# Kernel optimization log

Hardware: AMD Instinct MI355X
Metric: run time of the kernel (lower is better)

## Reference

```python
import jax, jax.numpy as jnp
import numpy as np

D = 256  # MCB sketch/output dimension


def count_sketch(x, h, s, d=D):
    # x: [B,H,W,C] channel-last; h: [C] int hash indices in [0,d); s: [C] +/-1 signs
    xs = x * s
    return jnp.zeros(x.shape[:-1] + (d,), x.dtype).at[..., h].add(xs)


def mcb(x, y, h1, s1, h2, s2, d=D):
    # Compact bilinear pooling per spatial location. x,y: [B,C,H,W] -> [B,d,H,W]
    xt = jnp.moveaxis(x, 1, -1)
    yt = jnp.moveaxis(y, 1, -1)
    fx = jnp.fft.rfft(count_sketch(xt, h1, s1, d), axis=-1)
    fy = jnp.fft.rfft(count_sketch(yt, h2, s2, d), axis=-1)
    out = jnp.fft.irfft(fx * fy, n=d, axis=-1)  # circular convolution of the two sketches
    return jnp.moveaxis(out, -1, 1)


def setup_inputs() -> dict:
    key = jax.random.key(0)
    ks = jax.random.split(key, 10)
    B, C, H, W, ATTR = 64, 256, 28, 28, 300
    entity_feature = jax.random.normal(ks[0], (B, C, H, W), jnp.float32)
    attr_one_hot = jax.random.uniform(ks[1], (B, ATTR), jnp.float32)
    W_emb = jax.random.normal(ks[2], (C, ATTR), jnp.float32) * 0.05
    b_emb = jax.random.normal(ks[3], (C,), jnp.float32) * 0.01
    h1 = jax.random.randint(ks[4], (C,), 0, D, jnp.int32)
    h2 = jax.random.randint(ks[5], (C,), 0, D, jnp.int32)
    s1 = jnp.where(jax.random.bernoulli(ks[6], 0.5, (C,)), 1.0, -1.0).astype(jnp.float32)
    s2 = jnp.where(jax.random.bernoulli(ks[7], 0.5, (C,)), 1.0, -1.0).astype(jnp.float32)
    conv1_w = jax.random.normal(ks[8], (32, C), jnp.float32) * 0.05
    conv2_w = jax.random.normal(ks[9], (1, 32), jnp.float32) * 0.05
    return {"entity_feature": entity_feature, "attr_one_hot": attr_one_hot,
            "W_emb": W_emb, "b_emb": b_emb, "h1": h1, "s1": s1, "h2": h2, "s2": s2,
            "conv1_w": conv1_w, "conv2_w": conv2_w}


def reference(entity_feature, attr_one_hot, W_emb, b_emb, h1, s1, h2, s2, conv1_w, conv2_w):
    # textual embedding: Linear(attr_num -> 256)
    emb = attr_one_hot @ W_emb.T + b_emb                      # [B,256]
    attr = jnp.broadcast_to(emb[:, :, None, None], entity_feature.shape)  # expand_as
    mcb_feat = mcb(attr, entity_feature, h1, s1, h2, s2)      # [B,256,H,W]
    hidden = jax.nn.relu(jnp.einsum('bchw,oc->bohw', mcb_feat, conv1_w))  # conv1x1 256->32
    attr_map = jax.nn.sigmoid(jnp.einsum('bchw,oc->bohw', hidden, conv2_w))  # conv1x1 32->1
    attr_feature = attr_map * entity_feature
    return attr_map, attr_feature
```

## Files before the change

### kernel.cpp

```cpp
#include <hip/hip_runtime.h>
#include <math.h>

#define BATCH 64
#define CC    256
#define ATTRN 300
#define DD    256
#define HW    784
#define HW4   196
#define O1    32
#define TF4   49


__global__ __launch_bounds__(256) void k1_emb_sketch(
    const float* __restrict__ attr_one_hot,
    const float* __restrict__ W_emb,
    const float* __restrict__ b_emb,
    const int*   __restrict__ h1,
    const float* __restrict__ s1,
    float* __restrict__ sx)
{
    const int b = blockIdx.x, t = threadIdx.x;
    __shared__ float s_attr[ATTRN];
    __shared__ float s_W[256 * 36];
    __shared__ float s_sx[DD];

    s_attr[t] = attr_one_hot[b * ATTRN + t];
    if (t < ATTRN - 256) s_attr[256 + t] = attr_one_hot[b * ATTRN + 256 + t];
    s_sx[t] = 0.f;

    float acc = b_emb[t];
    for (int a0 = 0; a0 < ATTRN; a0 += 32) {
        __syncthreads();
        const int ncol = (ATTRN - a0) < 32 ? (ATTRN - a0) : 32;
        const int nf4 = ncol >> 2;
        for (int i = t; i < 256 * nf4; i += 256) {
            int r = i / nf4, v = i - r * nf4;
            float4 w = *(const float4*)(W_emb + r * ATTRN + a0 + 4 * v);
            *(float4*)(&s_W[r * 36 + 4 * v]) = w;
        }
        __syncthreads();
        for (int v = 0; v < nf4; ++v) {
            float4 wv = *(const float4*)(&s_W[t * 36 + 4 * v]);
            float4 av = *(const float4*)(&s_attr[a0 + 4 * v]);
            acc += av.x * wv.x + av.y * wv.y + av.z * wv.z + av.w * wv.w;
        }
    }
    __syncthreads();
    atomicAdd(&s_sx[h1[t]], acc * s1[t]);
    __syncthreads();
    sx[b * DD + t] = s_sx[t];
}

__global__ __launch_bounds__(256) void k2_corr(
    const float* __restrict__ sx,
    const float* __restrict__ conv1_w,
    float* __restrict__ corrT)
{
    const int b = blockIdx.x, og = blockIdx.y, t = threadIdx.x;
    const int o0 = og * 8;
    __shared__ float s_sx[DD];
    __shared__ float s_w1[8][DD];
    __shared__ float s_c[8][DD];

    s_sx[t] = sx[b * DD + t];
#pragma unroll
    for (int j = 0; j < 8; ++j) s_w1[j][t] = conv1_w[(o0 + j) * CC + t];
    __syncthreads();

    float acc[8] = {0.f,0.f,0.f,0.f,0.f,0.f,0.f,0.f};
    for (int k4 = 0; k4 < 64; ++k4) {
        const int k = k4 * 4;
        float x0 = s_sx[(k     - t) & 255];
        float x1 = s_sx[(k + 1 - t) & 255];
        float x2 = s_sx[(k + 2 - t) & 255];
        float x3 = s_sx[(k + 3 - t) & 255];
#pragma unroll
        for (int oo = 0; oo < 8; ++oo) {
            float4 w = *(const float4*)&s_w1[oo][k];
            acc[oo] += w.x * x0 + w.y * x1 + w.z * x2 + w.w * x3;
        }
    }
#pragma unroll
    for (int oo = 0; oo < 8; ++oo) s_c[oo][t] = acc[oo];
    __syncthreads();

    float4 r0, r1;
    r0.x = s_c[0][t]; r0.y = s_c[1][t]; r0.z = s_c[2][t]; r0.w = s_c[3][t];
    r1.x = s_c[4][t]; r1.y = s_c[5][t]; r1.z = s_c[6][t]; r1.w = s_c[7][t];
    float4* dst = (float4*)(corrT + ((size_t)b * DD + t) * O1 + o0);
    dst[0] = r0; dst[1] = r1;
}

#define FMA4(A, S, E) { (A).x += (S)*(E).x; (A).y += (S)*(E).y; (A).z += (S)*(E).z; (A).w += (S)*(E).w; }

__global__ __launch_bounds__(1024, 4) void k3_main(
    const float* __restrict__ ent,
    const float* __restrict__ corrT,
    const int*   __restrict__ h2,
    const float* __restrict__ s2,
    const float* __restrict__ conv2_w,
    float* __restrict__ out_map,
    float* __restrict__ out_feat)
{
    const int b = blockIdx.x, tile = blockIdx.y;
    const int tid  = threadIdx.x;
    const int wv   = tid >> 6, lane = tid & 63;
    const int ci   = wv >> 2;
    const int oi   = wv & 3;

    union SMem {
        float  Pl[CC][36];
        float4 red[4][TF4][9];
    };
    __shared__ SMem sm;
    __shared__ float4 s_amap4[TF4];
    __shared__ float  s_c2[O1];

    {
        const int c = tid >> 2, qp = tid & 3;
        const int hc = h2[c];
        const float sc = s2[c];
        const float4* src = (const float4*)(corrT + ((size_t)b * DD + hc) * O1);
        float4 x0 = src[2 * qp], x1 = src[2 * qp + 1];
        x0.x *= sc; x0.y *= sc; x0.z *= sc; x0.w *= sc;
        x1.x *= sc; x1.y *= sc; x1.z *= sc; x1.w *= sc;
        *(float4*)&sm.Pl[c][8 * qp]     = x0;
        *(float4*)&sm.Pl[c][8 * qp + 4] = x1;
        if (tid < O1) s_c2[tid] = conv2_w[tid];
    }
    __syncthreads();

    const bool act = lane < TF4;
    const int f4i = tile * TF4 + (act ? lane : TF4 - 1);
    const float4* ent4 = (const float4*)ent;
    const int c0 = ci * 64;

    float4 acc[8];
#pragma unroll
    for (int o = 0; o < 8; ++o) acc[o] = make_float4(0.f, 0.f, 0.f, 0.f);

    const float4* eptr = ent4 + (size_t)(b * CC + c0) * HW4 + f4i;
#pragma unroll 4
    for (int cc = 0; cc < 64; ++cc) {
        const int c = c0 + cc;
        float4 e4 = eptr[(size_t)cc * HW4];
        float4 pa = *(const float4*)&sm.Pl[c][8 * oi];
        float4 pb = *(const float4*)&sm.Pl[c][8 * oi + 4];
        FMA4(acc[0], pa.x, e4); FMA4(acc[1], pa.y, e4);
        FMA4(acc[2], pa.z, e4); FMA4(acc[3], pa.w, e4);
        FMA4(acc[4], pb.x, e4); FMA4(acc[5], pb.y, e4);
        FMA4(acc[6], pb.z, e4); FMA4(acc[7], pb.w, e4);
    }

    float pre = 0.f;
#pragma unroll
    for (int g = 0; g < 4; ++g) {
        __syncthreads();
        if (oi == g && act) {
#pragma unroll
            for (int i = 0; i < 8; ++i) sm.red[ci][lane][i] = acc[i];
        }
        __syncthreads();
        if (tid < 4 * TF4) {
            const int fi = tid >> 2, j = tid & 3;
#pragma unroll
            for (int i = 0; i < 8; ++i) {
                float v = ((const float*)&sm.red[0][fi][i])[j]
                        + ((const float*)&sm.red[1][fi][i])[j]
                        + ((const float*)&sm.red[2][fi][i])[j]
                        + ((const float*)&sm.red[3][fi][i])[j];
                pre += s_c2[8 * g + i] * fmaxf(v, 0.f);
            }
        }
    }
    __syncthreads();
    if (tid < 4 * TF4) {
        const int fi = tid >> 2, j = tid & 3;
        float am = 1.f / (1.f + expf(-pre));
        ((float*)&s_amap4[fi])[j] = am;
        out_map[b * HW + tile * (4 * TF4) + tid] = am;
    }
    __syncthreads();

    const float4 am4 = s_amap4[act ? lane : 0];
    float4* of4 = (float4*)out_feat;
    const int cb = wv * 16;
#pragma unroll 4
    for (int cc = 0; cc < 16; ++cc) {
        const int c = cb + cc;
        if (act) {
            const size_t idx = (size_t)(b * CC + c) * HW4 + f4i;
            float4 e4 = ent4[idx];
            float4 r;
            r.x = am4.x * e4.x; r.y = am4.y * e4.y;
            r.z = am4.z * e4.z; r.w = am4.w * e4.w;
            of4[idx] = r;
        }
    }
}

extern "C" void kernel_launch(void* const* d_in, const int* in_sizes, int n_in,
                              void* d_out, int out_size, void* d_ws, size_t ws_size,
                              hipStream_t stream) {
    const float* ent   = (const float*)d_in[0];
    const float* attr  = (const float*)d_in[1];
    const float* W_emb = (const float*)d_in[2];
    const float* b_emb = (const float*)d_in[3];
    const int*   h1    = (const int*)d_in[4];
    const float* s1    = (const float*)d_in[5];
    const int*   h2    = (const int*)d_in[6];
    const float* s2    = (const float*)d_in[7];
    const float* c1w   = (const float*)d_in[8];
    const float* c2w   = (const float*)d_in[9];

    float* ws    = (float*)d_ws;
    float* sx    = ws;
    float* corrT = ws + 16384;

    float* out      = (float*)d_out;
    float* out_map  = out;
    float* out_feat = out + BATCH * HW;

    hipLaunchKernelGGL(k1_emb_sketch, dim3(BATCH), dim3(256), 0, stream,
                       attr, W_emb, b_emb, h1, s1, sx);
    hipLaunchKernelGGL(k2_corr, dim3(BATCH, 4), dim3(256), 0, stream,
                       sx, c1w, corrT);
    hipLaunchKernelGGL(k3_main, dim3(BATCH, 4), dim3(1024), 0, stream,
                       ent, corrT, h2, s2, c2w, out_map, out_feat);
}
```

Before: 185.6 us.

## Split embedding GEMV across more blocks, move sketch into corr kernel, batch loads in main loop

The embedding kernel now runs over (batch, 4) blocks, with four threads per output row reading W_emb directly and reducing through shuffles, in place of one block per batch staging W in shared memory. The count-sketch scatter moves into the correlation kernel, which now does its own shared-memory atomic add. In the main kernel, the channel loop issues eight entity float4 loads back to back, pinned by empty asm, before the FMAs, so more memory latency is in flight. The risks are higher register pressure under launch_bounds(1024,4) and the sketch being recomputed redundantly in each of the four output-group blocks.

```diff
diff --git a/kernel.cpp b/kernel.cpp
--- a/kernel.cpp
+++ b/kernel.cpp
@@ -11,48 +11,42 @@
 #define TF4   49
 
 
-__global__ __launch_bounds__(256) void k1_emb_sketch(
+__global__ __launch_bounds__(256) void k1_emb(
     const float* __restrict__ attr_one_hot,
     const float* __restrict__ W_emb,
     const float* __restrict__ b_emb,
+    float* __restrict__ emb)
+{
+    const int b = blockIdx.x, q = blockIdx.y, t = threadIdx.x;
+    __shared__ float s_attr[ATTRN];
+
+    if (t < 75) {
+        float4 a = *(const float4*)(attr_one_hot + b * ATTRN + 4 * t);
+        *(float4*)&s_attr[4 * t] = a;
+    }
+    __syncthreads();
+
+    const int r  = t >> 2, j = t & 3;
+    const int tr = q * 64 + r;
+    const int a0 = j * 76;
+    const int nf4 = (j == 3) ? 18 : 19;
+    const float* wr = W_emb + (size_t)tr * ATTRN + a0;
+
+    float acc = 0.f;
+    for (int v = 0; v < nf4; ++v) {
+        float4 w = *(const float4*)(wr + 4 * v);
+        float4 a = *(const float4*)(&s_attr[a0 + 4 * v]);
+        acc += w.x * a.x + w.y * a.y + w.z * a.z + w.w * a.w;
+    }
+    acc += __shfl_xor(acc, 1);
+    acc += __shfl_xor(acc, 2);
+    if (j == 0) emb[b * CC + tr] = acc + b_emb[tr];
+}
+
+__global__ __launch_bounds__(256) void k2_corr(
+    const float* __restrict__ emb,
     const int*   __restrict__ h1,
     const float* __restrict__ s1,
-    float* __restrict__ sx)
-{
-    const int b = blockIdx.x, t = threadIdx.x;
-    __shared__ float s_attr[ATTRN];
-    __shared__ float s_W[256 * 36];
-    __shared__ float s_sx[DD];
-
-    s_attr[t] = attr_one_hot[b * ATTRN + t];
-    if (t < ATTRN - 256) s_attr[256 + t] = attr_one_hot[b * ATTRN + 256 + t];
-    s_sx[t] = 0.f;
-
-    float acc = b_emb[t];
-    for (int a0 = 0; a0 < ATTRN; a0 += 32) {
-        __syncthreads();
-        const int ncol = (ATTRN - a0) < 32 ? (ATTRN - a0) : 32;
-        const int nf4 = ncol >> 2;
-        for (int i = t; i < 256 * nf4; i += 256) {
-            int r = i / nf4, v = i - r * nf4;
-            float4 w = *(const float4*)(W_emb + r * ATTRN + a0 + 4 * v);
-            *(float4*)(&s_W[r * 36 + 4 * v]) = w;
-        }
-        __syncthreads();
-        for (int v = 0; v < nf4; ++v) {
-            float4 wv = *(const float4*)(&s_W[t * 36 + 4 * v]);
-            float4 av = *(const float4*)(&s_attr[a0 + 4 * v]);
-            acc += av.x * wv.x + av.y * wv.y + av.z * wv.z + av.w * wv.w;
-        }
-    }
-    __syncthreads();
-    atomicAdd(&s_sx[h1[t]], acc * s1[t]);
-    __syncthreads();
-    sx[b * DD + t] = s_sx[t];
-}
-
-__global__ __launch_bounds__(256) void k2_corr(
-    const float* __restrict__ sx,
     const float* __restrict__ conv1_w,
     float* __restrict__ corrT)
 {
@@ -62,9 +56,11 @@
     __shared__ float s_w1[8][DD];
     __shared__ float s_c[8][DD];
 
-    s_sx[t] = sx[b * DD + t];
+    s_sx[t] = 0.f;
 #pragma unroll
     for (int j = 0; j < 8; ++j) s_w1[j][t] = conv1_w[(o0 + j) * CC + t];
+    __syncthreads();
+    atomicAdd(&s_sx[h1[t]], s1[t] * emb[b * CC + t]);
     __syncthreads();
 
     float acc[8] = {0.f,0.f,0.f,0.f,0.f,0.f,0.f,0.f};
@@ -140,16 +136,23 @@
     for (int o = 0; o < 8; ++o) acc[o] = make_float4(0.f, 0.f, 0.f, 0.f);
 
     const float4* eptr = ent4 + (size_t)(b * CC + c0) * HW4 + f4i;
-#pragma unroll 4
-    for (int cc = 0; cc < 64; ++cc) {
-        const int c = c0 + cc;
-        float4 e4 = eptr[(size_t)cc * HW4];
-        float4 pa = *(const float4*)&sm.Pl[c][8 * oi];
-        float4 pb = *(const float4*)&sm.Pl[c][8 * oi + 4];
-        FMA4(acc[0], pa.x, e4); FMA4(acc[1], pa.y, e4);
-        FMA4(acc[2], pa.z, e4); FMA4(acc[3], pa.w, e4);
-        FMA4(acc[4], pb.x, e4); FMA4(acc[5], pb.y, e4);
-        FMA4(acc[6], pb.z, e4); FMA4(acc[7], pb.w, e4);
+    for (int cc0 = 0; cc0 < 64; cc0 += 8) {
+        float4 e[8];
+#pragma unroll
+        for (int u = 0; u < 8; ++u) {
+            e[u] = eptr[(size_t)(cc0 + u) * HW4];
+            asm volatile("" : "+v"(e[u].x), "+v"(e[u].y), "+v"(e[u].z), "+v"(e[u].w));
+        }
+#pragma unroll
+        for (int u = 0; u < 8; ++u) {
+            const int c = c0 + cc0 + u;
+            float4 pa = *(const float4*)&sm.Pl[c][8 * oi];
+            float4 pb = *(const float4*)&sm.Pl[c][8 * oi + 4];
+            FMA4(acc[0], pa.x, e[u]); FMA4(acc[1], pa.y, e[u]);
+            FMA4(acc[2], pa.z, e[u]); FMA4(acc[3], pa.w, e[u]);
+            FMA4(acc[4], pb.x, e[u]); FMA4(acc[5], pb.y, e[u]);
+            FMA4(acc[6], pb.z, e[u]); FMA4(acc[7], pb.w, e[u]);
+        }
     }
 
     float pre = 0.f;
@@ -214,17 +217,17 @@
     const float* c2w   = (const float*)d_in[9];
 
     float* ws    = (float*)d_ws;
-    float* sx    = ws;
+    float* emb   = ws;
     float* corrT = ws + 16384;
 
     float* out      = (float*)d_out;
     float* out_map  = out;
     float* out_feat = out + BATCH * HW;
 
-    hipLaunchKernelGGL(k1_emb_sketch, dim3(BATCH), dim3(256), 0, stream,
-                       attr, W_emb, b_emb, h1, s1, sx);
+    hipLaunchKernelGGL(k1_emb, dim3(BATCH, 4), dim3(256), 0, stream,
+                       attr, W_emb, b_emb, emb);
     hipLaunchKernelGGL(k2_corr, dim3(BATCH, 4), dim3(256), 0, stream,
-                       sx, c1w, corrT);
+                       emb, h1, s1, c1w, corrT);
     hipLaunchKernelGGL(k3_main, dim3(BATCH, 4), dim3(1024), 0, stream,
                        ent, corrT, h2, s2, c2w, out_map, out_feat);
 }
```

New measurement: 169.5 us. 1.09x faster.

## Fuse embedding sketch into correlation kernel and split k-loop across two thread halves

Applied to the files above, without the earlier changes.

Merges the embedding/count-sketch kernel into the circular-correlation kernel, so each block recomputes the 256-wide embedding for its batch instead of writing it to a workspace and launching a second kernel. The block doubles to 512 threads: one half loads attr and computes the embedding by reading W_emb rows directly from global memory without shared-memory staging, while the other half loads conv1 weights. The correlation k-loop is then split in two and combined through shared memory. This removes one launch and a global round trip, but the embedding matvec is now computed redundantly by the four output-group blocks per batch, and the uncoalesced per-thread row reads of W_emb may be slow.

```diff
diff --git a/kernel.cpp b/kernel.cpp
--- a/kernel.cpp
+++ b/kernel.cpp
@@ -11,65 +11,54 @@
 #define TF4   49
 
 
-__global__ __launch_bounds__(256) void k1_emb_sketch(
+__global__ __launch_bounds__(512) void k2_fused(
     const float* __restrict__ attr_one_hot,
     const float* __restrict__ W_emb,
     const float* __restrict__ b_emb,
     const int*   __restrict__ h1,
     const float* __restrict__ s1,
-    float* __restrict__ sx)
-{
-    const int b = blockIdx.x, t = threadIdx.x;
-    __shared__ float s_attr[ATTRN];
-    __shared__ float s_W[256 * 36];
-    __shared__ float s_sx[DD];
-
-    s_attr[t] = attr_one_hot[b * ATTRN + t];
-    if (t < ATTRN - 256) s_attr[256 + t] = attr_one_hot[b * ATTRN + 256 + t];
-    s_sx[t] = 0.f;
-
-    float acc = b_emb[t];
-    for (int a0 = 0; a0 < ATTRN; a0 += 32) {
-        __syncthreads();
-        const int ncol = (ATTRN - a0) < 32 ? (ATTRN - a0) : 32;
-        const int nf4 = ncol >> 2;
-        for (int i = t; i < 256 * nf4; i += 256) {
-            int r = i / nf4, v = i - r * nf4;
-            float4 w = *(const float4*)(W_emb + r * ATTRN + a0 + 4 * v);
-            *(float4*)(&s_W[r * 36 + 4 * v]) = w;
-        }
-        __syncthreads();
-        for (int v = 0; v < nf4; ++v) {
-            float4 wv = *(const float4*)(&s_W[t * 36 + 4 * v]);
-            float4 av = *(const float4*)(&s_attr[a0 + 4 * v]);
-            acc += av.x * wv.x + av.y * wv.y + av.z * wv.z + av.w * wv.w;
-        }
-    }
-    __syncthreads();
-    atomicAdd(&s_sx[h1[t]], acc * s1[t]);
-    __syncthreads();
-    sx[b * DD + t] = s_sx[t];
-}
-
-__global__ __launch_bounds__(256) void k2_corr(
-    const float* __restrict__ sx,
     const float* __restrict__ conv1_w,
     float* __restrict__ corrT)
 {
-    const int b = blockIdx.x, og = blockIdx.y, t = threadIdx.x;
+    const int b = blockIdx.x, og = blockIdx.y;
+    const int tid = threadIdx.x;
+    const int t = tid & 255, kh = tid >> 8;
     const int o0 = og * 8;
+
+    __shared__ float s_attr[ATTRN];
     __shared__ float s_sx[DD];
     __shared__ float s_w1[8][DD];
-    __shared__ float s_c[8][DD];
-
-    s_sx[t] = sx[b * DD + t];
-#pragma unroll
-    for (int j = 0; j < 8; ++j) s_w1[j][t] = conv1_w[(o0 + j) * CC + t];
+    __shared__ float s_part[8][DD];
+
+    if (kh == 0) {
+        s_sx[t] = 0.f;
+        if (t < 75) {
+            float4 a = *(const float4*)(attr_one_hot + b * ATTRN + 4 * t);
+            *(float4*)&s_attr[4 * t] = a;
+        }
+    } else {
+#pragma unroll
+        for (int j = 0; j < 8; ++j) s_w1[j][t] = conv1_w[(o0 + j) * CC + t];
+    }
+    __syncthreads();
+
+    if (kh == 0) {
+        float acc = b_emb[t];
+        const float* wr = W_emb + (size_t)t * ATTRN;
+#pragma unroll 5
+        for (int v = 0; v < 75; ++v) {
+            float4 w = *(const float4*)(wr + 4 * v);
+            float4 a = *(const float4*)(&s_attr[4 * v]);
+            acc += w.x * a.x + w.y * a.y + w.z * a.z + w.w * a.w;
+        }
+        atomicAdd(&s_sx[h1[t]], s1[t] * acc);
+    }
     __syncthreads();
 
     float acc[8] = {0.f,0.f,0.f,0.f,0.f,0.f,0.f,0.f};
-    for (int k4 = 0; k4 < 64; ++k4) {
-        const int k = k4 * 4;
+    const int kbase = kh << 7;
+    for (int k4 = 0; k4 < 32; ++k4) {
+        const int k = kbase + 4 * k4;
         float x0 = s_sx[(k     - t) & 255];
         float x1 = s_sx[(k + 1 - t) & 255];
         float x2 = s_sx[(k + 2 - t) & 255];
@@ -80,15 +69,20 @@
             acc[oo] += w.x * x0 + w.y * x1 + w.z * x2 + w.w * x3;
         }
     }
-#pragma unroll
-    for (int oo = 0; oo < 8; ++oo) s_c[oo][t] = acc[oo];
-    __syncthreads();
-
-    float4 r0, r1;
-    r0.x = s_c[0][t]; r0.y = s_c[1][t]; r0.z = s_c[2][t]; r0.w = s_c[3][t];
-    r1.x = s_c[4][t]; r1.y = s_c[5][t]; r1.z = s_c[6][t]; r1.w = s_c[7][t];
-    float4* dst = (float4*)(corrT + ((size_t)b * DD + t) * O1 + o0);
-    dst[0] = r0; dst[1] = r1;
+    if (kh == 1) {
+#pragma unroll
+        for (int oo = 0; oo < 8; ++oo) s_part[oo][t] = acc[oo];
+    }
+    __syncthreads();
+    if (kh == 0) {
+        float4 r0, r1;
+        r0.x = acc[0] + s_part[0][t]; r0.y = acc[1] + s_part[1][t];
+        r0.z = acc[2] + s_part[2][t]; r0.w = acc[3] + s_part[3][t];
+        r1.x = acc[4] + s_part[4][t]; r1.y = acc[5] + s_part[5][t];
+        r1.z = acc[6] + s_part[6][t]; r1.w = acc[7] + s_part[7][t];
+        float4* dst = (float4*)(corrT + ((size_t)b * DD + t) * O1 + o0);
+        dst[0] = r0; dst[1] = r1;
+    }
 }
 
 #define FMA4(A, S, E) { (A).x += (S)*(E).x; (A).y += (S)*(E).y; (A).z += (S)*(E).z; (A).w += (S)*(E).w; }
@@ -214,17 +208,14 @@
     const float* c2w   = (const float*)d_in[9];
 
     float* ws    = (float*)d_ws;
-    float* sx    = ws;
     float* corrT = ws + 16384;
 
     float* out      = (float*)d_out;
     float* out_map  = out;
     float* out_feat = out + BATCH * HW;
 
-    hipLaunchKernelGGL(k1_emb_sketch, dim3(BATCH), dim3(256), 0, stream,
-                       attr, W_emb, b_emb, h1, s1, sx);
-    hipLaunchKernelGGL(k2_corr, dim3(BATCH, 4), dim3(256), 0, stream,
-                       sx, c1w, corrT);
+    hipLaunchKernelGGL(k2_fused, dim3(BATCH, 4), dim3(512), 0, stream,
+                       attr, W_emb, b_emb, h1, s1, c1w, corrT);
     hipLaunchKernelGGL(k3_main, dim3(BATCH, 4), dim3(1024), 0, stream,
                        ent, corrT, h2, s2, c2w, out_map, out_feat);
 }
```

Measured after the change: 156.9 us. 1.18x faster.
